# Kernel optimization log

Hardware: AMD Instinct MI355X
Metric: run time of the kernel (lower is better)

## Reference

```python
import jax, jax.numpy as jnp
import numpy as np
import math


def ste_round(x):
    # round with straight-through gradient (identity in bwd)
    return x + jax.lax.stop_gradient(jnp.round(x) - x)


def ste_floor(x):
    return x + jax.lax.stop_gradient(jnp.floor(x) - x)


def _conv(x, w, b):
    # 5x5 stride-2 conv, padding=2 (kernel_size//2), NCHW/OIHW
    y = jax.lax.conv_general_dilated(
        x, w, window_strides=(2, 2), padding=[(2, 2), (2, 2)],
        dimension_numbers=('NCHW', 'OIHW', 'NCHW'))
    return y + b[None, :, None, None]


def _split_conv(x, w, b_int, mul, split=4):
    # 4 redundant sub-convolutions with floor-STE quantized integer weights/biases
    wq = ste_round(w)  # wSTE: round-to-int with STE
    out = 0.0
    for i in range(split):
        out = out + _conv(x, ste_floor((wq + i) / split), ste_floor((b_int + i) / split))
    return out * mul[None, :, None, None]


def _forward(x, w0, b0, w1, b1, w2, b2, w3, b3, mul0, mul1, mul2, mul3,
             relu0, relu1, relu2, md0, md1, md2, md3, ga_left):
    Bits = 8; clp_k = 8; in_scale = 8; scl_k = 3
    relus = [relu0, relu1, relu2]
    clp = [round((2 ** Bits - 1) / r * 2 ** (16 + clp_k)) for r in relus]
    scl = [math.floor((r + 2 ** (scl_k - 1)) / 2 ** scl_k) for r in relus]

    # quantize input to uint8 range
    x = jnp.clip(ste_round(x * 2 ** in_scale), 0, 255)

    # ---- layer 0 ----
    x = _split_conv(x, w0, ste_round(b0 * 2 ** in_scale), mul0)
    x = ste_floor((x + 2.0 ** (md0 - 1 + in_scale - clp_k)) / 2.0 ** (md0 + in_scale - clp_k))
    x = jnp.clip(x, 0, clp[0])
    x = ste_floor((ste_round(x * scl[0]) + 2.0 ** (15 + clp_k - scl_k)) / 2.0 ** (16 + clp_k - scl_k))

    # ---- layers 1, 2 ----
    for w_, b_, mul_, md_, idx in ((w1, b1, mul1, md1, 1), (w2, b2, mul2, md2, 2)):
        x = _split_conv(x, w_, ste_round(b_), mul_)
        x = ste_floor((x + 2.0 ** (md_ - 1 - clp_k)) / 2.0 ** (md_ - clp_k))
        x = jnp.clip(x, 0, clp[idx])
        x = ste_floor((ste_round(x * scl[idx]) + 2.0 ** (15 + clp_k - scl_k)) / 2.0 ** (16 + clp_k - scl_k))

    # ---- layer 3 (latent) ----
    x = _split_conv(x, w3, ste_round(b3), mul3)
    x = ste_floor((x + 2.0 ** (md3 - 1 - ga_left)) / 2.0 ** (md3 - ga_left))
    return x


def setup_inputs():
    key = jax.random.key(0)
    ks = jax.random.split(key, 16)
    N, M = 192, 320
    d = {}
    d['x'] = jax.random.uniform(ks[0], (4, 3, 512, 512), dtype=jnp.float32)
    # float weights whose round() gives small ints (integerized LIC weights)
    d['w0'] = jax.random.normal(ks[1], (N, 3, 5, 5), dtype=jnp.float32) * 3.0
    d['b0'] = jax.random.normal(ks[2], (N,), dtype=jnp.float32)
    d['w1'] = jax.random.normal(ks[3], (N, N, 5, 5), dtype=jnp.float32) * 3.0
    d['b1'] = jax.random.normal(ks[4], (N,), dtype=jnp.float32) * 16.0
    d['w2'] = jax.random.normal(ks[5], (N, N, 5, 5), dtype=jnp.float32) * 3.0
    d['b2'] = jax.random.normal(ks[6], (N,), dtype=jnp.float32) * 16.0
    d['w3'] = jax.random.normal(ks[7], (M, N, 5, 5), dtype=jnp.float32) * 3.0
    d['b3'] = jax.random.normal(ks[8], (M,), dtype=jnp.float32) * 16.0
    # per-channel integer-valued fixed-point multipliers
    d['mul0'] = jax.random.randint(ks[9], (N,), 1, 64).astype(jnp.float32)
    d['mul1'] = jax.random.randint(ks[10], (N,), 1, 64).astype(jnp.float32)
    d['mul2'] = jax.random.randint(ks[11], (N,), 1, 64).astype(jnp.float32)
    d['mul3'] = jax.random.randint(ks[12], (M,), 1, 64).astype(jnp.float32)
    d['relu0'] = 65536; d['relu1'] = 65536; d['relu2'] = 65536
    d['md0'] = 7; d['md1'] = 15; d['md2'] = 15; d['md3'] = 10
    d['ga_left'] = 4
    return d


def reference(x, w0, b0, w1, b1, w2, b2, w3, b3, mul0, mul1, mul2, mul3,
              relu0, relu1, relu2, md0, md1, md2, md3, ga_left):
    return _forward(x, w0, b0, w1, b1, w2, b2, w3, b3, mul0, mul1, mul2, mul3,
                    relu0, relu1, relu2, md0, md1, md2, md3, ga_left)
```

## Files before the change

### kernel.cpp

```cpp
#include <hip/hip_runtime.h>
#include <hip/hip_bf16.h>

typedef int i32x4 __attribute__((ext_vector_type(4)));
typedef unsigned int u32;
typedef unsigned long long u64;
typedef long long ll;

__device__ __forceinline__ void load_lds16(const void* g, void* l) {
  __builtin_amdgcn_global_load_lds(
      (const __attribute__((address_space(1))) u32*)g,
      (__attribute__((address_space(3))) u32*)l, 16, 0, 0);
}

__global__ __launch_bounds__(256) void prep_all(
    const float* __restrict__ w0, const float* __restrict__ w1,
    const float* __restrict__ w2, const float* __restrict__ w3,
    signed char* __restrict__ w0q, signed char* __restrict__ w1p,
    signed char* __restrict__ w2p, signed char* __restrict__ w3p,
    signed char* __restrict__ zbuf,
    int* __restrict__ totw0, int* __restrict__ totw1,
    int* __restrict__ totw2, int* __restrict__ totw3)
{
  __shared__ signed char ldsw[8 * 4800];
  const int blk = blockIdx.x;
  const int tid = threadIdx.x;

  if (blk < 88) {
    const float* wsrc; signed char* wdst; int* tot; int MF, sub;
    if (blk < 24)      { wsrc = w1; wdst = w1p; tot = totw1; MF = 12; sub = blk; }
    else if (blk < 48) { wsrc = w2; wdst = w2p; tot = totw2; MF = 12; sub = blk - 24; }
    else               { wsrc = w3; wdst = w3p; tot = totw3; MF = 20; sub = blk - 48; }
    const int mf = sub >> 1, half = sub & 1, colbase = half * 8;
    const int ocb = mf * 16 + colbase;
    for (int o = 0; o < 8; o++) {
      const float* src = wsrc + (size_t)(ocb + o) * 4800;
      int s = 0;
      for (int j = tid; j < 4800; j += 256) {
        int v = (int)rintf(src[j]);
        ldsw[o * 4800 + j] = (signed char)v;
        s += v;
      }
      atomicAdd(&tot[ocb + o], s);
    }
    __syncthreads();
    for (int u = tid; u < 9600; u += 256) {
      int eu = u & 3, colL = (u >> 2) & 7, q = (u >> 5) & 3, t = u >> 7;
      int tap = t / 3, ch = t - 3 * tap;
      int ci0 = ch * 64 + q * 16 + eu * 4;
      const signed char* sp = ldsw + colL * 4800 + tap;
      u32 wv = 0;
      #pragma unroll
      for (int bb = 0; bb < 4; bb++)
        wv |= ((u32)(unsigned char)sp[(ci0 + bb) * 25]) << (8 * bb);
      *(u32*)(wdst + ((size_t)t * MF + mf) * 1024 +
              (q * 16 + colbase + colL) * 16 + eu * 4) = wv;
    }
  } else {
    if (tid < 128) ((u64*)zbuf)[tid] = 0x8080808080808080ULL;
    for (int i = tid; i < 24576; i += 256) {
      int e = i & 15, colA = (i >> 4) & 15, q = (i >> 8) & 3, t = i >> 10;
      int mf = t % 12, ch = t / 12;
      signed char v = 0;
      if (e < 15 && (ch == 0 || q == 0)) {
        int ky = (ch == 0) ? q : 4;
        int ci = e / 5, kx = e - ci * 5;
        v = (signed char)(int)rintf(
            w0[((mf * 16 + colA) * 3 + ci) * 25 + ky * 5 + kx]);
      }
      w0q[i] = v;
    }
    for (int oc = tid; oc < 192; oc += 256) {
      const float* p = w0 + (size_t)oc * 75;
      int s = 0;
      #pragma unroll 5
      for (int j = 0; j < 75; j++) s += (int)rintf(p[j]);
      totw0[oc] = s;
    }
  }
}

__global__ __launch_bounds__(192, 3) void conv0F(
    const float* __restrict__ x, const signed char* __restrict__ wq,
    const float* __restrict__ bias, const float* __restrict__ mulv,
    const int* __restrict__ totw,
    const int* __restrict__ reluP, const int* __restrict__ mdP,
    unsigned char* __restrict__ outA)
{
  __shared__ signed char ilds[3][5][132];

  const int tid = threadIdx.x;
  const int lane = tid & 63;
  const int col = lane & 15;
  const int quad = lane >> 4;
  const int w = tid >> 6;
  const int blk = blockIdx.x;
  const int oxblk = blk & 3;
  const int oy = (blk >> 2) & 255;
  const int b = blk >> 10;
  const int oxbase = oxblk * 64;

  i32x4 afr[2][4];
  #pragma unroll
  for (int ch = 0; ch < 2; ch++)
    #pragma unroll
    for (int i = 0; i < 4; i++)
      afr[ch][i] = *(const i32x4*)(wq + ch * 12288 + (w * 4 + i) * 1024 + lane * 16);

  const float* xb = x + (size_t)b * 3 * 512 * 512;
  for (int i = tid; i < 990; i += 192) {
    int j = i % 66; int t = i / 66; int r = t % 5; int ci = t / 5;
    int iy = 2 * oy - 2 + r;
    int ix = 2 * oxbase - 2 + 2 * j;
    int v0 = -128, v1 = -128;
    if ((unsigned)iy < 512u) {
      const float* row = xb + ((size_t)ci * 512 + iy) * 512;
      if ((unsigned)ix < 512u) {
        float xv = rintf(row[ix] * 256.0f);
        v0 = (int)fminf(fmaxf(xv, 0.0f), 255.0f) - 128;
      }
      if ((unsigned)(ix + 1) < 512u) {
        float xv = rintf(row[ix + 1] * 256.0f);
        v1 = (int)fminf(fmaxf(xv, 0.0f), 255.0f) - 128;
      }
    }
    *(unsigned short*)&ilds[ci][r][2 * j] =
        (unsigned short)((v0 & 0xFF) | ((v1 & 0xFF) << 8));
  }
  __syncthreads();

  i32x4 acc[4][4];
  #pragma unroll
  for (int fm = 0; fm < 4; fm++)
    #pragma unroll
    for (int fn = 0; fn < 4; fn++) acc[fm][fn] = (i32x4){0, 0, 0, 0};

  #pragma unroll
  for (int ch = 0; ch < 2; ch++) {
    const int row = (ch == 0) ? quad : 4;
    i32x4 bfr[4];
    #pragma unroll
    for (int fn = 0; fn < 4; fn++) {
      const int xb2 = 2 * (fn * 16 + col);
      const int o8 = (xb2 & 3) * 8;
      const int ab = xb2 & ~3;
      u64 w0_, w1_, w2_;
      {
        const u32* p0 = (const u32*)&ilds[0][row][ab];
        const u32* p1 = (const u32*)&ilds[1][row][ab];
        const u32* p2 = (const u32*)&ilds[2][row][ab];
        w0_ = (u64)p0[0] | ((u64)p0[1] << 32);
        w1_ = (u64)p1[0] | ((u64)p1[1] << 32);
        w2_ = (u64)p2[0] | ((u64)p2[1] << 32);
      }
      u32 a0 = (u32)(w0_ >> o8);
      u32 a1 = ((u32)(w0_ >> (o8 + 32)) & 0xFFu) | (((u32)(w1_ >> o8)) << 8);
      u32 a2 = ((u32)(w1_ >> (o8 + 24)) & 0xFFFFu) | (((u32)(w2_ >> o8)) << 16);
      u32 a3 = (u32)(w2_ >> (o8 + 16));
      bfr[fn] = (i32x4){(int)a0, (int)a1, (int)a2, (int)a3};
    }
    #pragma unroll
    for (int fm = 0; fm < 4; fm++)
      #pragma unroll
      for (int fn = 0; fn < 4; fn++)
        acc[fm][fn] = __builtin_amdgcn_mfma_i32_16x16x64_i8(
            afr[ch][fm], bfr[fn], acc[fm][fn], 0, 0, 0);
  }

  const size_t pix0 = ((size_t)(b * 256 + oy)) * 256 + oxbase;
  const int rl = reluP[0];
  const int sh = mdP[0];
  const ll clpv_ll = llrint(255.0 / (double)rl * 16777216.0);
  const int clpv = clpv_ll > 0x7FFFFFFFLL ? 0x7FFFFFFF : (int)clpv_ll;
  const int sclv = (int)((rl + 4) >> 3);
  const int rnd = 1 << (sh - 1);
  #pragma unroll
  for (int fm = 0; fm < 4; fm++) {
    const int oc0 = w * 64 + fm * 16 + quad * 4;
    int bim[4], mu32[4];
    #pragma unroll
    for (int r = 0; r < 4; r++) {
      int bi = (int)llrintf(bias[oc0 + r] * 256.0f) + 128 * totw[oc0 + r];
      mu32[r] = (int)llrintf(mulv[oc0 + r]);
      bim[r] = bi * mu32[r];
    }
    #pragma unroll
    for (int fn = 0; fn < 4; fn++) {
      const size_t pix = pix0 + fn * 16 + col;
      u32 wd = 0;
      #pragma unroll
      for (int r = 0; r < 4; r++) {
        int vi = acc[fm][fn][r] * mu32[r] + bim[r];
        int y = (vi + rnd) >> sh;
        y = y < 0 ? 0 : (y > clpv ? clpv : y);
        y = (y * sclv + (1 << 20)) >> 21;
        wd |= (((u32)y ^ 0x80u) & 0xFFu) << (8 * r);
      }
      *(u32*)(outA + pix * 192 + oc0) = wd;
    }
  }
}

template <int COUT, int HIN, int WIN, int HOUT, int WOUT, int MW,
          int KSPLIT, bool DIRECT>
__global__ __launch_bounds__(MW * 64, 3) void convS(
    const signed char* __restrict__ act, const signed char* __restrict__ wp,
    const float* __restrict__ bias, const float* __restrict__ mulv,
    const int* __restrict__ totw,
    const int* __restrict__ reluP, const int* __restrict__ mdP,
    const signed char* __restrict__ zbuf,
    unsigned char* __restrict__ outA, int* __restrict__ outP)
{
  constexpr int CIN = 192;
  constexpr int PASSES = 4;
  constexpr int MAXP = (PASSES + MW - 1) / MW;
  constexpr int SAe = MW * 4096;
  constexpr int TX = WOUT / 16;
  constexpr int TYB = HOUT / 4;
  constexpr int TPP = 25 / KSPLIT;
  constexpr int NSTEP = TPP * 3;
  constexpr int PSZ = 4 * HOUT * WOUT * COUT;
  static_assert(MW * 64 == COUT, "M covers COUT");

  __shared__ __align__(16) char smem[2 * 4096];

  const int tid = threadIdx.x;
  const int lane = tid & 63;
  const int col = lane & 15;
  const int quad = lane >> 4;
  const int w = tid >> 6;
  const int part = blockIdx.y;

  int bx = blockIdx.x;
  const int tx = bx % TX; bx /= TX;
  const int ty = bx % TYB;
  const int b = bx / TYB;
  const int ox0 = tx * 16;
  const int oy0 = ty * 4;

  const signed char* bptr[MAXP];
  int bmx[MAXP], bmy[MAXP];
  #pragma unroll
  for (int k = 0; k < MAXP; k++) {
    int p = w + k * MW;
    if (p >= PASSES) break;
    int oxv = ox0 + col;
    int oyv = oy0 + p;
    bptr[k] = act + ((size_t)b * HIN * WIN + (size_t)(2 * oyv) * WIN + 2 * oxv) * CIN
              + quad * 16;
    int mx = 0, my = 0;
    #pragma unroll
    for (int kk = 0; kk < 5; kk++) {
      if ((unsigned)(2 * oxv + kk - 2) < (unsigned)WIN) mx |= 1 << kk;
      if ((unsigned)(2 * oyv + kk - 2) < (unsigned)HIN) my |= 1 << kk;
    }
    bmx[k] = mx; bmy[k] = my;
  }

  int kxS, kyS, chS;

  auto stage = [&](int sel) {
    const int offB = ((kyS - 2) * WIN + (kxS - 2)) * CIN + chS * 64;
    #pragma unroll
    for (int k = 0; k < MAXP; k++) {
      int p = w + k * MW;
      if (p >= PASSES) break;
      bool v = ((bmx[k] >> kxS) & 1) && ((bmy[k] >> kyS) & 1);
      const signed char* g = v ? (bptr[k] + offB) : (zbuf + quad * 16);
      load_lds16(g, smem + sel * 4096 + p * 1024);
    }
  };
  auto adv = [&]() {
    chS++;
    if (chS == 3) { chS = 0; kxS++; if (kxS == 5) { kxS = 0; kyS++; } }
  };

  i32x4 acc[4][4];
  #pragma unroll
  for (int fm = 0; fm < 4; fm++)
    #pragma unroll
    for (int fn = 0; fn < 4; fn++) acc[fm][fn] = (i32x4){0, 0, 0, 0};

  const int tap0 = part * TPP;
  kyS = tap0 / 5; kxS = tap0 - 5 * kyS; chS = 0;
  stage(0);
  adv();
  const signed char* aptr = wp + (size_t)(tap0 * 3) * SAe + w * 4096 + lane * 16;
  i32x4 aA[4], aB[4];
  #pragma unroll
  for (int i = 0; i < 4; i++) aA[i] = *(const i32x4*)(aptr + i * 1024);

  auto comp = [&](int base, i32x4 (&a)[4]) {
    const char* pB = smem + base + lane * 16;
    i32x4 bfr[4];
    #pragma unroll
    for (int i = 0; i < 4; i++)
      bfr[i] = *(const i32x4*)(pB + i * 1024);
    #pragma unroll
    for (int fm = 0; fm < 4; fm++)
      #pragma unroll
      for (int fn = 0; fn < 4; fn++)
        acc[fm][fn] = __builtin_amdgcn_mfma_i32_16x16x64_i8(
            a[fm], bfr[fn], acc[fm][fn], 0, 0, 0);
  };

  int sl = 0;
  #pragma unroll 1
  for (; sl + 1 < NSTEP; sl += 2) {
    __syncthreads();
    stage(1); adv();
    aptr += SAe;
    #pragma unroll
    for (int i = 0; i < 4; i++) aB[i] = *(const i32x4*)(aptr + i * 1024);
    comp(0, aA);

    __syncthreads();
    if (sl + 2 < NSTEP) {
      stage(0); adv();
      aptr += SAe;
      #pragma unroll
      for (int i = 0; i < 4; i++) aA[i] = *(const i32x4*)(aptr + i * 1024);
    }
    comp(4096, aB);
  }
  if (sl < NSTEP) {
    __syncthreads();
    comp(0, aA);
  }

  if constexpr (DIRECT) {
    const int rl = reluP[0];
    const int sh = mdP[0] - 8;
    const ll clpv = llrint(255.0 / (double)rl * 16777216.0);
    const ll sclv = (ll)((rl + 4) >> 3);
    #pragma unroll
    for (int fm = 0; fm < 4; fm++) {
      const int oc0 = w * 64 + fm * 16 + quad * 4;
      ll bi[4], mu[4];
      #pragma unroll
      for (int r = 0; r < 4; r++) {
        bi[r] = llrintf(bias[oc0 + r]) + 128LL * totw[oc0 + r];
        mu[r] = llrintf(mulv[oc0 + r]);
      }
      #pragma unroll
      for (int fn = 0; fn < 4; fn++) {
        const int oyv = oy0 + fn;
        const int oxv = ox0 + col;
        u32 wd = 0;
        #pragma unroll
        for (int r = 0; r < 4; r++) {
          ll vi = ((ll)acc[fm][fn][r] + bi[r]) * mu[r];
          ll y = (vi + (1LL << (sh - 1))) >> sh;
          y = y < 0 ? 0LL : (y > clpv ? clpv : y);
          y = (y * sclv + (1LL << 20)) >> 21;
          wd |= (((u32)y ^ 0x80u) & 0xFFu) << (8 * r);
        }
        *(u32*)(outA + ((size_t)((b * HOUT + oyv) * WOUT + oxv)) * COUT + oc0) = wd;
      }
    }
  } else {
    int* pout = outP + (size_t)part * PSZ;
    #pragma unroll
    for (int fm = 0; fm < 4; fm++) {
      const int oc0 = w * 64 + fm * 16 + quad * 4;
      #pragma unroll
      for (int fn = 0; fn < 4; fn++) {
        const int oyv = oy0 + fn;
        const int oxv = ox0 + col;
        *(i32x4*)(pout + ((size_t)((b * HOUT + oyv) * WOUT + oxv)) * COUT + oc0) =
            acc[fm][fn];
      }
    }
  }
}

__global__ __launch_bounds__(256) void reduce2(
    const int* __restrict__ partP, const float* __restrict__ bias,
    const float* __restrict__ mulv, const int* __restrict__ totw,
    const int* __restrict__ reluP, const int* __restrict__ mdP,
    unsigned char* __restrict__ outA)
{
  const int gid = blockIdx.x * 256 + threadIdx.x;
  const int PSZ4 = 4 * 64 * 64 * 192 / 4;
  const int4* pp = (const int4*)partP;
  int4 sv = pp[gid];
  #pragma unroll
  for (int p = 1; p < 5; p++) {
    int4 v = pp[(size_t)p * PSZ4 + gid];
    sv.x += v.x; sv.y += v.y; sv.z += v.z; sv.w += v.w;
  }
  int sa[4] = {sv.x, sv.y, sv.z, sv.w};
  const int oc0 = (gid * 4) % 192;
  const int rl = reluP[0];
  const int sh = mdP[0] - 8;
  const ll clpv = llrint(255.0 / (double)rl * 16777216.0);
  const ll sclv = (ll)((rl + 4) >> 3);
  u32 wd = 0;
  #pragma unroll
  for (int r = 0; r < 4; r++) {
    ll bi = llrintf(bias[oc0 + r]) + 128LL * totw[oc0 + r];
    ll mu = llrintf(mulv[oc0 + r]);
    ll vi = ((ll)sa[r] + bi) * mu;
    ll y = (vi + (1LL << (sh - 1))) >> sh;
    y = y < 0 ? 0LL : (y > clpv ? clpv : y);
    y = (y * sclv + (1LL << 20)) >> 21;
    wd |= (((u32)y ^ 0x80u) & 0xFFu) << (8 * r);
  }
  ((u32*)outA)[gid] = wd;
}

__global__ __launch_bounds__(256) void reduce3(
    const int* __restrict__ partP, const float* __restrict__ b3,
    const float* __restrict__ mul3, const int* __restrict__ totw3,
    const int* __restrict__ mdP, const int* __restrict__ gaP,
    float* __restrict__ outF)
{
  const int gid = blockIdx.x * 256 + threadIdx.x;
  int t = gid;
  const int ox = t & 31; t >>= 5;
  const int oy = t & 31; t >>= 5;
  const int oc = t % 320;
  const int b  = t / 320;
  const int PSZ = 4 * 32 * 32 * 320;
  const size_t src = ((size_t)((b * 32 + oy) * 32 + ox)) * 320 + oc;
  ll s = 0;
  #pragma unroll
  for (int p = 0; p < 5; p++) s += partP[(size_t)p * PSZ + src];
  const int sh = mdP[0] - gaP[0];
  const ll bi = llrintf(b3[oc]) + 128LL * totw3[oc];
  const ll mu = llrintf(mul3[oc]);
  const ll y = ((s + bi) * mu + (1LL << (sh - 1))) >> sh;
  outF[gid] = (float)y;
}

extern "C" void kernel_launch(void* const* d_in, const int* in_sizes, int n_in,
                              void* d_out, int out_size, void* d_ws, size_t ws_size,
                              hipStream_t stream)
{
  const float* x    = (const float*)d_in[0];
  const float* w0   = (const float*)d_in[1];
  const float* b0   = (const float*)d_in[2];
  const float* w1   = (const float*)d_in[3];
  const float* b1   = (const float*)d_in[4];
  const float* w2   = (const float*)d_in[5];
  const float* b2   = (const float*)d_in[6];
  const float* w3   = (const float*)d_in[7];
  const float* b3   = (const float*)d_in[8];
  const float* mul0 = (const float*)d_in[9];
  const float* mul1 = (const float*)d_in[10];
  const float* mul2 = (const float*)d_in[11];
  const float* mul3 = (const float*)d_in[12];
  const int* relu0  = (const int*)d_in[13];
  const int* relu1  = (const int*)d_in[14];
  const int* relu2  = (const int*)d_in[15];
  const int* md0    = (const int*)d_in[16];
  const int* md1    = (const int*)d_in[17];
  const int* md2    = (const int*)d_in[18];
  const int* md3    = (const int*)d_in[19];
  const int* ga     = (const int*)d_in[20];

  char* ws = (char*)d_ws;
  size_t off = 0;
  signed char* zbuf = (signed char*)(ws + off); off += 1024;
  signed char* w0q  = (signed char*)(ws + off); off += 24576;
  signed char* w1p  = (signed char*)(ws + off); off += 921600;
  signed char* w2p  = (signed char*)(ws + off); off += 921600;
  signed char* w3p  = (signed char*)(ws + off); off += 1536000;
  int*         totw1= (int*)        (ws + off); off += 192 * 4;
  int*         totw2= (int*)        (ws + off); off += 192 * 4;
  int*         totw3= (int*)        (ws + off); off += 320 * 4;
  int*         totw0= (int*)        (ws + off); off += 192 * 4;
  unsigned char* act1 = (unsigned char*)(ws + off); off += (size_t)4 * 256 * 256 * 192;
  unsigned char* act2 = (unsigned char*)(ws + off); off += (size_t)4 * 128 * 128 * 192;
  unsigned char* act3 = (unsigned char*)(ws + off); off += (size_t)4 * 64 * 64 * 192;
  int*         partl  = (int*)(ws + off); off += (size_t)5 * 4 * 64 * 64 * 192 * 4;
  (void)ws_size; (void)in_sizes; (void)n_in; (void)out_size;

  hipMemsetAsync(totw1, 0, (192 + 192 + 320 + 192) * 4, stream);
  prep_all<<<89, 256, 0, stream>>>(w0, w1, w2, w3, w0q, w1p, w2p, w3p,
                                   zbuf, totw0, totw1, totw2, totw3);
  conv0F<<<4096, 192, 0, stream>>>(x, w0q, b0, mul0, totw0, relu0, md0, act1);
  convS<192, 256, 256, 128, 128, 3, 1, true><<<dim3(1024, 1), 192, 0, stream>>>(
      (const signed char*)act1, w1p, b1, mul1, totw1, relu1, md1, zbuf, act2, nullptr);
  convS<192, 128, 128, 64, 64, 3, 5, false><<<dim3(256, 5), 192, 0, stream>>>(
      (const signed char*)act2, w2p, b2, mul2, totw2, relu2, md2, zbuf, nullptr, partl);
  reduce2<<<3072, 256, 0, stream>>>(partl, b2, mul2, totw2, relu2, md2, act3);
  convS<320, 64, 64, 32, 32, 5, 5, false><<<dim3(64, 5), 320, 0, stream>>>(
      (const signed char*)act3, w3p, b3, mul3, totw3, nullptr, md3, zbuf, nullptr, partl);
  reduce3<<<5120, 256, 0, stream>>>(partl, b3, mul3, totw3, md3, ga, (float*)d_out);
}
```

Baseline: 348.5 us.

## Split convS into single-wave blocks per 64-channel slice, replace barriers with waitcnt

Each convS block now holds one wavefront that computes one 64-output-channel slice over a 4x16 pixel tile. The grid multiplies by COUT/64 and the per-wave role split inside the block is removed. Because a single wave stages its own LDS tile, __syncthreads is replaced by explicit vmcnt waits around the async global-to-LDS loads, with scheduling barriers to keep the order. The cost is that each block re-stages the activation tile, so activation traffic from L2 grows by the channel-split factor, in exchange for no block barriers and more independent waves.

```diff
diff --git a/kernel.cpp b/kernel.cpp
--- a/kernel.cpp
+++ b/kernel.cpp
@@ -11,6 +11,9 @@
       (const __attribute__((address_space(1))) u32*)g,
       (__attribute__((address_space(3))) u32*)l, 16, 0, 0);
 }
+
+#define WAITCNT_VM8 0x3FF8
+#define WAITCNT_VM0 0x3FF0
 
 __global__ __launch_bounds__(256) void prep_all(
     const float* __restrict__ w0, const float* __restrict__ w1,
@@ -200,9 +203,8 @@
   }
 }
 
-template <int COUT, int HIN, int WIN, int HOUT, int WOUT, int MW,
-          int KSPLIT, bool DIRECT>
-__global__ __launch_bounds__(MW * 64, 3) void convS(
+template <int COUT, int HIN, int WIN, int HOUT, int WOUT, int KSPLIT, bool DIRECT>
+__global__ __launch_bounds__(64, 4) void convS(
     const signed char* __restrict__ act, const signed char* __restrict__ wp,
     const float* __restrict__ bias, const float* __restrict__ mulv,
     const int* __restrict__ totw,
@@ -211,61 +213,58 @@
     unsigned char* __restrict__ outA, int* __restrict__ outP)
 {
   constexpr int CIN = 192;
-  constexpr int PASSES = 4;
-  constexpr int MAXP = (PASSES + MW - 1) / MW;
-  constexpr int SAe = MW * 4096;
+  constexpr int MF = COUT / 16;
+  constexpr int SAe = MF * 1024;
+  constexpr int OCT = COUT / 64;
   constexpr int TX = WOUT / 16;
   constexpr int TYB = HOUT / 4;
   constexpr int TPP = 25 / KSPLIT;
   constexpr int NSTEP = TPP * 3;
   constexpr int PSZ = 4 * HOUT * WOUT * COUT;
-  static_assert(MW * 64 == COUT, "M covers COUT");
+  constexpr int ROWST = 2 * WIN * CIN;
 
   __shared__ __align__(16) char smem[2 * 4096];
 
-  const int tid = threadIdx.x;
-  const int lane = tid & 63;
+  const int lane = threadIdx.x;
   const int col = lane & 15;
   const int quad = lane >> 4;
-  const int w = tid >> 6;
   const int part = blockIdx.y;
 
   int bx = blockIdx.x;
+  const int oct = bx % OCT; bx /= OCT;
   const int tx = bx % TX; bx /= TX;
   const int ty = bx % TYB;
   const int b = bx / TYB;
   const int ox0 = tx * 16;
   const int oy0 = ty * 4;
 
-  const signed char* bptr[MAXP];
-  int bmx[MAXP], bmy[MAXP];
-  #pragma unroll
-  for (int k = 0; k < MAXP; k++) {
-    int p = w + k * MW;
-    if (p >= PASSES) break;
-    int oxv = ox0 + col;
+  const int oxv = ox0 + col;
+  const signed char* bbase =
+      act + ((size_t)b * HIN * WIN + (size_t)(2 * oy0) * WIN + 2 * oxv) * CIN
+      + quad * 16;
+  int bmx = 0;
+  #pragma unroll
+  for (int kk = 0; kk < 5; kk++)
+    if ((unsigned)(2 * oxv + kk - 2) < (unsigned)WIN) bmx |= 1 << kk;
+  u32 bmyP = 0;
+  #pragma unroll
+  for (int p = 0; p < 4; p++) {
     int oyv = oy0 + p;
-    bptr[k] = act + ((size_t)b * HIN * WIN + (size_t)(2 * oyv) * WIN + 2 * oxv) * CIN
-              + quad * 16;
-    int mx = 0, my = 0;
-    #pragma unroll
-    for (int kk = 0; kk < 5; kk++) {
-      if ((unsigned)(2 * oxv + kk - 2) < (unsigned)WIN) mx |= 1 << kk;
+    u32 my = 0;
+    #pragma unroll
+    for (int kk = 0; kk < 5; kk++)
       if ((unsigned)(2 * oyv + kk - 2) < (unsigned)HIN) my |= 1 << kk;
-    }
-    bmx[k] = mx; bmy[k] = my;
-  }
+    bmyP |= my << (8 * p);
+  }
+  const signed char* zp = zbuf + quad * 16;
 
   int kxS, kyS, chS;
-
   auto stage = [&](int sel) {
     const int offB = ((kyS - 2) * WIN + (kxS - 2)) * CIN + chS * 64;
     #pragma unroll
-    for (int k = 0; k < MAXP; k++) {
-      int p = w + k * MW;
-      if (p >= PASSES) break;
-      bool v = ((bmx[k] >> kxS) & 1) && ((bmy[k] >> kyS) & 1);
-      const signed char* g = v ? (bptr[k] + offB) : (zbuf + quad * 16);
+    for (int p = 0; p < 4; p++) {
+      bool v = ((bmx >> kxS) & 1) && ((bmyP >> (8 * p + kyS)) & 1);
+      const signed char* g = v ? (bbase + p * ROWST + offB) : zp;
       load_lds16(g, smem + sel * 4096 + p * 1024);
     }
   };
@@ -282,12 +281,12 @@
 
   const int tap0 = part * TPP;
   kyS = tap0 / 5; kxS = tap0 - 5 * kyS; chS = 0;
-  stage(0);
-  adv();
-  const signed char* aptr = wp + (size_t)(tap0 * 3) * SAe + w * 4096 + lane * 16;
+  stage(0); adv();
+  const signed char* aptr = wp + (size_t)(tap0 * 3) * SAe + oct * 4096 + lane * 16;
   i32x4 aA[4], aB[4];
   #pragma unroll
   for (int i = 0; i < 4; i++) aA[i] = *(const i32x4*)(aptr + i * 1024);
+  aptr += SAe;
 
   auto comp = [&](int base, i32x4 (&a)[4]) {
     const char* pB = smem + base + lane * 16;
@@ -303,29 +302,29 @@
             a[fm], bfr[fn], acc[fm][fn], 0, 0, 0);
   };
 
-  int sl = 0;
   #pragma unroll 1
-  for (; sl + 1 < NSTEP; sl += 2) {
-    __syncthreads();
+  for (int sl = 0; sl < NSTEP; sl += 2) {
     stage(1); adv();
+    #pragma unroll
+    for (int i = 0; i < 4; i++) aB[i] = *(const i32x4*)(aptr + i * 1024);
     aptr += SAe;
-    #pragma unroll
-    for (int i = 0; i < 4; i++) aB[i] = *(const i32x4*)(aptr + i * 1024);
+    __builtin_amdgcn_sched_barrier(0);
+    __builtin_amdgcn_s_waitcnt(WAITCNT_VM8);
+    __builtin_amdgcn_sched_barrier(0);
     comp(0, aA);
 
-    __syncthreads();
-    if (sl + 2 < NSTEP) {
+    if (sl + 1 < NSTEP) {
       stage(0); adv();
+      #pragma unroll
+      for (int i = 0; i < 4; i++) aA[i] = *(const i32x4*)(aptr + i * 1024);
       aptr += SAe;
-      #pragma unroll
-      for (int i = 0; i < 4; i++) aA[i] = *(const i32x4*)(aptr + i * 1024);
-    }
-    comp(4096, aB);
-  }
-  if (sl < NSTEP) {
-    __syncthreads();
-    comp(0, aA);
-  }
+      __builtin_amdgcn_sched_barrier(0);
+      __builtin_amdgcn_s_waitcnt(WAITCNT_VM8);
+      __builtin_amdgcn_sched_barrier(0);
+      comp(4096, aB);
+    }
+  }
+  __builtin_amdgcn_s_waitcnt(WAITCNT_VM0);
 
   if constexpr (DIRECT) {
     const int rl = reluP[0];
@@ -334,7 +333,7 @@
     const ll sclv = (ll)((rl + 4) >> 3);
     #pragma unroll
     for (int fm = 0; fm < 4; fm++) {
-      const int oc0 = w * 64 + fm * 16 + quad * 4;
+      const int oc0 = oct * 64 + fm * 16 + quad * 4;
       ll bi[4], mu[4];
       #pragma unroll
       for (int r = 0; r < 4; r++) {
@@ -344,7 +343,6 @@
       #pragma unroll
       for (int fn = 0; fn < 4; fn++) {
         const int oyv = oy0 + fn;
-        const int oxv = ox0 + col;
         u32 wd = 0;
         #pragma unroll
         for (int r = 0; r < 4; r++) {
@@ -361,11 +359,10 @@
     int* pout = outP + (size_t)part * PSZ;
     #pragma unroll
     for (int fm = 0; fm < 4; fm++) {
-      const int oc0 = w * 64 + fm * 16 + quad * 4;
+      const int oc0 = oct * 64 + fm * 16 + quad * 4;
       #pragma unroll
       for (int fn = 0; fn < 4; fn++) {
         const int oyv = oy0 + fn;
-        const int oxv = ox0 + col;
         *(i32x4*)(pout + ((size_t)((b * HOUT + oyv) * WOUT + oxv)) * COUT + oc0) =
             acc[fm][fn];
       }
@@ -479,12 +476,12 @@
   prep_all<<<89, 256, 0, stream>>>(w0, w1, w2, w3, w0q, w1p, w2p, w3p,
                                    zbuf, totw0, totw1, totw2, totw3);
   conv0F<<<4096, 192, 0, stream>>>(x, w0q, b0, mul0, totw0, relu0, md0, act1);
-  convS<192, 256, 256, 128, 128, 3, 1, true><<<dim3(1024, 1), 192, 0, stream>>>(
+  convS<192, 256, 256, 128, 128, 1, true><<<dim3(3072, 1), 64, 0, stream>>>(
       (const signed char*)act1, w1p, b1, mul1, totw1, relu1, md1, zbuf, act2, nullptr);
-  convS<192, 128, 128, 64, 64, 3, 5, false><<<dim3(256, 5), 192, 0, stream>>>(
+  convS<192, 128, 128, 64, 64, 5, false><<<dim3(768, 5), 64, 0, stream>>>(
       (const signed char*)act2, w2p, b2, mul2, totw2, relu2, md2, zbuf, nullptr, partl);
   reduce2<<<3072, 256, 0, stream>>>(partl, b2, mul2, totw2, relu2, md2, act3);
-  convS<320, 64, 64, 32, 32, 5, 5, false><<<dim3(64, 5), 320, 0, stream>>>(
+  convS<320, 64, 64, 32, 32, 5, false><<<dim3(320, 5), 64, 0, stream>>>(
       (const signed char*)act3, w3p, b3, mul3, totw3, nullptr, md3, zbuf, nullptr, partl);
   reduce3<<<5120, 256, 0, stream>>>(partl, b3, mul3, totw3, md3, ga, (float*)d_out);
 }
```

Result: slower. 470.8 us (+35.1%).
